# Kernel tuning notes

Hardware: AMD Instinct MI355X
Metric: run time of the kernel (lower is better)

Reference implementation:

```python
import jax, jax.numpy as jnp
import numpy as np

D = 1024

def setup_inputs() -> dict:
    key = jax.random.key(0)
    ks = jax.random.split(key, 16)
    B, S = 8, 2048
    s = 1.0 / np.sqrt(D)
    inp = {
        "visual_feat": jax.random.normal(ks[0], (B, S, D), jnp.float32),
        "audio_feat": jax.random.normal(ks[1], (B, S, D), jnp.float32),
        "Wq": jax.random.normal(ks[2], (D, D), jnp.float32) * s,
        "bq": jnp.zeros((D,), jnp.float32),
        "Wk": jax.random.normal(ks[3], (D, D), jnp.float32) * s,
        "bk": jnp.zeros((D,), jnp.float32),
        "Wv": jax.random.normal(ks[4], (D, D), jnp.float32) * s,
        "bv": jnp.zeros((D,), jnp.float32),
        "Wo": jax.random.normal(ks[5], (D, D), jnp.float32) * s,
        "bo": jnp.zeros((D,), jnp.float32),
        "W1": jax.random.normal(ks[6], (D, D), jnp.float32) * s,
        "b1": jnp.zeros((D,), jnp.float32),
        "W2": jax.random.normal(ks[7], (D, 1), jnp.float32) * s,
        "b2": jnp.zeros((1,), jnp.float32),
    }
    return inp

def reference(visual_feat, audio_feat, Wq, bq, Wk, bk, Wv, bv, Wo, bo, W1, b1, W2, b2):
    # Cross-modal attention: query from visual, key/value from audio.
    q = jnp.einsum('bsd,de->bse', visual_feat, Wq) + bq
    k = jnp.einsum('bsd,de->bse', audio_feat, Wk) + bk
    v = jnp.einsum('bsd,de->bse', audio_feat, Wv) + bv
    # NOTE: original has NO 1/sqrt(d) scaling — faithful to source.
    scores = jnp.einsum('bqe,bke->bqk', q, k)          # [B, S, S]
    attn = jax.nn.softmax(scores, axis=-1)
    attended = jnp.einsum('bqk,bke->bqe', attn, v)     # [B, S, D]
    attended = jnp.einsum('bse,ef->bsf', attended, Wo) + bo
    h = attended + visual_feat                          # residual
    x = jax.nn.relu(jnp.einsum('bsd,de->bse', h, W1) + b1)
    out = jnp.einsum('bsd,do->bso', x, W2) + b2        # [B, S, 1]
    return out
```

## Files before the change

kernel.cpp:

```cpp
#include <hip/hip_runtime.h>
#include <cstdint>
#include <cstddef>

typedef _Float16 f16;
typedef _Float16 f16x8 __attribute__((ext_vector_type(8)));
typedef _Float16 f16x4 __attribute__((ext_vector_type(4)));
typedef float    f32x4 __attribute__((ext_vector_type(4)));

#define AS1 __attribute__((address_space(1)))
#define AS3 __attribute__((address_space(3)))

static constexpr int BB = 8;
static constexpr int SS = 2048;
static constexpr int DD = 1024;
static constexpr int MTOT = BB * SS;

__global__ __launch_bounds__(256) void cast_f32_f16(const float* __restrict__ src,
                                                    f16* __restrict__ dst, int n4) {
  int i = blockIdx.x * 256 + threadIdx.x;
  if (i < n4) {
    const float4 f = reinterpret_cast<const float4*>(src)[i];
    f16x4 o = { (f16)f.x, (f16)f.y, (f16)f.z, (f16)f.w };
    reinterpret_cast<f16x4*>(dst)[i] = o;
  }
}

__global__ __launch_bounds__(256) void transpose_cast_wt(const float* __restrict__ W,
                                                         f16* __restrict__ WT, int D) {
  __shared__ float tile[32][33];
  const int bx = blockIdx.x * 32;
  const int by = blockIdx.y * 32;
  const int tx = threadIdx.x & 31;
  const int ty = threadIdx.x >> 5;
  for (int i = ty; i < 32; i += 8) tile[i][tx] = W[(size_t)(by + i) * D + bx + tx];
  __syncthreads();
  for (int i = ty; i < 32; i += 8)
    WT[(size_t)(bx + i) * D + by + tx] = (f16)tile[tx][i];
}

__global__ __launch_bounds__(256) void transpose_f16_batch(const f16* __restrict__ src,
                                                           f16* __restrict__ dst,
                                                           int R, int C) {
  __shared__ f16 tile[32][33];
  src += (size_t)blockIdx.z * R * C;
  dst += (size_t)blockIdx.z * R * C;
  const int bx = blockIdx.x * 32;
  const int by = blockIdx.y * 32;
  const int tx = threadIdx.x & 31;
  const int ty = threadIdx.x >> 5;
  for (int i = ty; i < 32; i += 8) tile[i][tx] = src[(size_t)(by + i) * C + bx + tx];
  __syncthreads();
  for (int i = ty; i < 32; i += 8) dst[(size_t)(bx + i) * R + by + tx] = tile[tx][i];
}

template <int EPI>
__global__ __launch_bounds__(512, 2) void gemm8(
    const f16* __restrict__ A, const f16* __restrict__ BT, void* __restrict__ Cout,
    const float* __restrict__ bias, const float* __restrict__ resid,
    int N, int K, int gx,
    size_t Abat, size_t Bbat, size_t Cbat) {
  __shared__ f16 smA[2][256 * 64];
  __shared__ f16 smB[2][256 * 64];

  const int bz = blockIdx.z;
  A += (size_t)bz * Abat;
  BT += (size_t)bz * Bbat;

  const int nwg = gridDim.x;
  const int q = nwg >> 3, r = nwg & 7;
  const int xcd = blockIdx.x & 7, lin = blockIdx.x >> 3;
  const int wg = (xcd < r ? xcd * (q + 1) : r * (q + 1) + (xcd - r) * q) + lin;
  const int n0 = (wg % gx) * 256;
  const int m0 = (wg / gx) * 256;

  const int tid = threadIdx.x;
  const int w = tid >> 6, lane = tid & 63;
  const int wr = w >> 2, wc = w & 3;
  const int lg = lane >> 4, lr = lane & 15;
  const int nt = K >> 6;

  f32x4 acc[8][4] = {};
  f16x8 alo[4][2], ahi[4][2], bfr[2][2];

  auto stageA = [&](int t, int h, int d) {
#pragma unroll
    for (int l = 0; l < 2; ++l) {
      const int cb = l * 512 + w * 64;
      const int c = cb + lane;
      const int rr = c >> 3;
      const int g = (c & 7) ^ (rr & 7);
      const f16* src = A + (size_t)(m0 + h * 128 + rr) * K + t * 64 + g * 8;
      __builtin_amdgcn_global_load_lds((const AS1 void*)src,
          (AS3 void*)(&smA[d][(h * 1024 + cb) * 8]), 16, 0, 0);
    }
  };
  auto stageB = [&](int t, int h, int d) {
#pragma unroll
    for (int l = 0; l < 2; ++l) {
      const int cb = l * 512 + w * 64;
      const int c = cb + lane;
      const int rr = c >> 3;
      const int g = (c & 7) ^ (rr & 7);
      const f16* src = BT + (size_t)(n0 + h * 128 + rr) * K + t * 64 + g * 8;
      __builtin_amdgcn_global_load_lds((const AS1 void*)src,
          (AS3 void*)(&smB[d][(h * 1024 + cb) * 8]), 16, 0, 0);
    }
  };
  auto lda = [&](f16x8 (&dst)[4][2], int mh, int d) {
#pragma unroll
    for (int i = 0; i < 4; ++i) {
      const int rrow = wr * 128 + (mh * 4 + i) * 16 + lr;
#pragma unroll
      for (int kh = 0; kh < 2; ++kh) {
        const int kg = (kh * 4 + lg) ^ (rrow & 7);
        dst[i][kh] = *(const f16x8*)(&smA[d][rrow * 64 + kg * 8]);
      }
    }
  };
  auto ldb = [&](int nh, int d) {
#pragma unroll
    for (int j = 0; j < 2; ++j) {
      const int nrow = wc * 64 + (nh * 2 + j) * 16 + lr;
#pragma unroll
      for (int kh = 0; kh < 2; ++kh) {
        const int kg = (kh * 4 + lg) ^ (nrow & 7);
        bfr[j][kh] = *(const f16x8*)(&smB[d][nrow * 64 + kg * 8]);
      }
    }
  };
  auto mma = [&](const f16x8 (&a)[4][2], int mh, int nh) {
#pragma unroll
    for (int i = 0; i < 4; ++i)
#pragma unroll
      for (int j = 0; j < 2; ++j)
#pragma unroll
        for (int kh = 0; kh < 2; ++kh)
          acc[mh * 4 + i][nh * 2 + j] = __builtin_amdgcn_mfma_f32_16x16x32_f16(
              a[i][kh], bfr[j][kh], acc[mh * 4 + i][nh * 2 + j], 0, 0, 0);
  };

#define PH_MID()                                                     \
  __builtin_amdgcn_sched_barrier(0);                                 \
  __builtin_amdgcn_s_barrier();                                      \
  asm volatile("s_waitcnt lgkmcnt(0)" ::: "memory");                 \
  __builtin_amdgcn_sched_barrier(0);                                 \
  __builtin_amdgcn_s_setprio(1)
#define PH_END()                                                     \
  __builtin_amdgcn_s_setprio(0);                                     \
  __builtin_amdgcn_sched_barrier(0);                                 \
  __builtin_amdgcn_s_barrier()
#define PH_END_VM4()                                                 \
  __builtin_amdgcn_s_setprio(0);                                     \
  asm volatile("s_waitcnt vmcnt(4)" ::: "memory");                   \
  __builtin_amdgcn_sched_barrier(0);                                 \
  __builtin_amdgcn_s_barrier()
#define PH_END_VM0()                                                 \
  __builtin_amdgcn_s_setprio(0);                                     \
  asm volatile("s_waitcnt vmcnt(0)" ::: "memory");                   \
  __builtin_amdgcn_sched_barrier(0);                                 \
  __builtin_amdgcn_s_barrier()

  stageA(0, 0, 0); stageA(0, 1, 0);
  stageB(0, 0, 0); stageB(0, 1, 0);
  if (nt > 1) { stageA(1, 0, 1); stageA(1, 1, 1); }
  asm volatile("s_waitcnt vmcnt(4)" ::: "memory");
  __builtin_amdgcn_sched_barrier(0);
  __builtin_amdgcn_s_barrier();

  for (int t = 0; t < nt; t += 2) {
    const int u = t + 1;
    const bool pok = (t + 2 < nt);
    lda(alo, 0, 0); ldb(0, 0); stageB(u, 0, 1);
    PH_MID(); mma(alo, 0, 0); PH_END();
    lda(ahi, 1, 0); stageB(u, 1, 1);
    PH_MID(); mma(ahi, 1, 0); PH_END();
    ldb(1, 0); if (pok) stageA(t + 2, 0, 0);
    PH_MID(); mma(ahi, 1, 1); PH_END();
    if (pok) stageA(t + 2, 1, 0);
    PH_MID(); mma(alo, 0, 1);
    if (pok) { PH_END_VM4(); } else { PH_END_VM0(); }
    lda(alo, 0, 1); ldb(0, 1); if (pok) stageB(t + 2, 0, 0);
    PH_MID(); mma(alo, 0, 0); PH_END();
    lda(ahi, 1, 1); if (pok) stageB(t + 2, 1, 0);
    PH_MID(); mma(ahi, 1, 0); PH_END();
    ldb(1, 1); if (pok) stageA(t + 3, 0, 1);
    PH_MID(); mma(ahi, 1, 1); PH_END();
    if (pok) stageA(t + 3, 1, 1);
    PH_MID(); mma(alo, 0, 1);
    if (pok) { PH_END_VM4(); } else { PH_END(); }
  }
#undef PH_MID
#undef PH_END
#undef PH_END_VM4
#undef PH_END_VM0

#pragma unroll
  for (int I = 0; I < 8; ++I) {
    const int row = m0 + wr * 128 + I * 16 + lg * 4;
#pragma unroll
    for (int J = 0; J < 4; ++J) {
      const int col = n0 + wc * 64 + J * 16 + lr;
      float bval = 0.f;
      if (EPI == 0 || EPI == 3 || EPI == 4) bval = bias[col];
#pragma unroll
      for (int rr = 0; rr < 4; ++rr) {
        float v = acc[I][J][rr] + bval;
        const size_t idx = (size_t)(row + rr) * N + col;
        if (EPI == 3) v += resid[idx];
        if (EPI == 4) v = fmaxf(v, 0.f);
        if (EPI == 1)
          ((float*)Cout)[(size_t)bz * Cbat + idx] = v;
        else
          ((f16*)Cout)[(size_t)bz * Cbat + idx] = (f16)v;
      }
    }
  }
}

__global__ __launch_bounds__(256) void softmax_rows(const float* __restrict__ Sc,
                                                    f16* __restrict__ P) {
  const size_t row = blockIdx.x;
  const float* x = Sc + row * SS;
  f16* p = P + row * SS;
  const int t = threadIdx.x;
  const int wid = t >> 6, lane = t & 63;
  __shared__ float red[8];

  float v[8];
  float mx = -3.4e38f;
#pragma unroll
  for (int i = 0; i < 8; ++i) {
    v[i] = x[t + i * 256];
    mx = fmaxf(mx, v[i]);
  }
#pragma unroll
  for (int o = 32; o >= 1; o >>= 1) mx = fmaxf(mx, __shfl_xor(mx, o));
  if (lane == 0) red[wid] = mx;
  __syncthreads();
  mx = fmaxf(fmaxf(red[0], red[1]), fmaxf(red[2], red[3]));

  float sum = 0.f;
#pragma unroll
  for (int i = 0; i < 8; ++i) {
    v[i] = __expf(v[i] - mx);
    sum += v[i];
  }
#pragma unroll
  for (int o = 32; o >= 1; o >>= 1) sum += __shfl_xor(sum, o);
  if (lane == 0) red[4 + wid] = sum;
  __syncthreads();
  sum = red[4] + red[5] + red[6] + red[7];
  const float inv = 1.0f / sum;
#pragma unroll
  for (int i = 0; i < 8; ++i) p[t + i * 256] = (f16)(v[i] * inv);
}

__global__ __launch_bounds__(256) void matvec_out(const f16* __restrict__ X,
                                                  const float* __restrict__ W2,
                                                  const float* __restrict__ b2,
                                                  float* __restrict__ out) {
  const int row = blockIdx.x * 4 + (threadIdx.x >> 6);
  const int lane = threadIdx.x & 63;
  const f16* x = X + (size_t)row * DD;
  float s = 0.f;
#pragma unroll
  for (int c = 0; c < 2; ++c) {
    const int base = lane * 8 + c * 512;
    f16x8 v = *(const f16x8*)(x + base);
#pragma unroll
    for (int e = 0; e < 8; ++e) s += (float)v[e] * W2[base + e];
  }
#pragma unroll
  for (int o = 32; o >= 1; o >>= 1) s += __shfl_xor(s, o);
  if (lane == 0) out[row] = s + b2[0];
}

extern "C" void kernel_launch(void* const* d_in, const int* in_sizes, int n_in,
                              void* d_out, int out_size, void* d_ws, size_t ws_size,
                              hipStream_t stream) {
  const float* vis = (const float*)d_in[0];
  const float* aud = (const float*)d_in[1];
  const float* Wq = (const float*)d_in[2];
  const float* bq = (const float*)d_in[3];
  const float* Wk = (const float*)d_in[4];
  const float* bk = (const float*)d_in[5];
  const float* Wv = (const float*)d_in[6];
  const float* bv = (const float*)d_in[7];
  const float* Wo = (const float*)d_in[8];
  const float* bo = (const float*)d_in[9];
  const float* W1 = (const float*)d_in[10];
  const float* b1 = (const float*)d_in[11];
  const float* W2 = (const float*)d_in[12];
  const float* b2 = (const float*)d_in[13];
  float* out = (float*)d_out;
  (void)in_sizes; (void)n_in; (void)out_size;

  char* ws = (char*)d_ws;
  size_t off = 0;
  auto carve = [&](size_t bytes) -> void* {
    void* p = ws + off;
    off += (bytes + 255) & ~(size_t)255;
    return p;
  };
  const size_t wtB = (size_t)DD * DD * sizeof(f16);
  const size_t bufB = (size_t)MTOT * DD * sizeof(f16);
  f16* WqT = (f16*)carve(wtB);
  f16* WkT = (f16*)carve(wtB);
  f16* WvT = (f16*)carve(wtB);
  f16* WoT = (f16*)carve(wtB);
  f16* W1T = (f16*)carve(wtB);
  f16* slot1 = (f16*)carve(bufB);
  f16* slot2 = (f16*)carve(bufB);
  f16* slot3 = (f16*)carve(bufB);
  f16* slot4 = (f16*)carve(bufB);

  const size_t rem = (ws_size > off) ? ws_size - off : 0;
  const size_t perBatch = (size_t)SS * SS * 6 + 512;
  int nb = 0;
  for (int c : {8, 4, 2, 1})
    if ((size_t)c * perBatch <= rem) { nb = c; break; }
  int RB = 0;
  if (!nb) {
    for (int r : {1024, 512, 256})
      if ((size_t)r * SS * 6 + 512 <= rem) { RB = r; break; }
    if (!RB) RB = 256;
  }

  f16* VIS16 = slot1;
  f16* AUD16 = slot2;
  f16* Q16 = slot3;
  f16* K16 = slot4;
  f16* V16 = slot1;
  f16* VT16 = slot2;
  f16* ATT16 = slot1;
  f16* H16 = slot2;
  f16* X16 = slot3;

  const dim3 blk(256);
  const dim3 blk8(512);
  const int n4 = MTOT * DD / 4;

  cast_f32_f16<<<dim3((n4 + 255) / 256), blk, 0, stream>>>(vis, VIS16, n4);
  cast_f32_f16<<<dim3((n4 + 255) / 256), blk, 0, stream>>>(aud, AUD16, n4);

  transpose_cast_wt<<<dim3(DD / 32, DD / 32), blk, 0, stream>>>(Wq, WqT, DD);
  transpose_cast_wt<<<dim3(DD / 32, DD / 32), blk, 0, stream>>>(Wk, WkT, DD);
  transpose_cast_wt<<<dim3(DD / 32, DD / 32), blk, 0, stream>>>(Wv, WvT, DD);
  transpose_cast_wt<<<dim3(DD / 32, DD / 32), blk, 0, stream>>>(Wo, WoT, DD);
  transpose_cast_wt<<<dim3(DD / 32, DD / 32), blk, 0, stream>>>(W1, W1T, DD);

  gemm8<0><<<dim3(4 * 64, 1, 1), blk8, 0, stream>>>(
      VIS16, WqT, Q16, bq, nullptr, DD, DD, 4, 0, 0, 0);
  gemm8<0><<<dim3(4 * 64, 1, 1), blk8, 0, stream>>>(
      AUD16, WkT, K16, bk, nullptr, DD, DD, 4, 0, 0, 0);
  gemm8<0><<<dim3(4 * 64, 1, 1), blk8, 0, stream>>>(
      AUD16, WvT, V16, bv, nullptr, DD, DD, 4, 0, 0, 0);

  transpose_f16_batch<<<dim3(DD / 32, SS / 32, BB), blk, 0, stream>>>(V16, VT16, SS, DD);

  if (nb) {
    float* S32 = (float*)carve((size_t)nb * SS * SS * sizeof(float));
    f16* Pc = (f16*)carve((size_t)nb * SS * SS * sizeof(f16));
    for (int b = 0; b < BB; b += nb) {
      gemm8<1><<<dim3((SS / 256) * (SS / 256), 1, nb), blk8, 0, stream>>>(
          Q16 + (size_t)b * SS * DD, K16 + (size_t)b * SS * DD, S32, nullptr, nullptr,
          SS, DD, SS / 256, (size_t)SS * DD, (size_t)SS * DD, (size_t)SS * SS);
      softmax_rows<<<dim3(nb * SS), blk, 0, stream>>>(S32, Pc);
      gemm8<2><<<dim3((DD / 256) * (SS / 256), 1, nb), blk8, 0, stream>>>(
          Pc, VT16 + (size_t)b * DD * SS, ATT16 + (size_t)b * SS * DD, nullptr, nullptr,
          DD, SS, DD / 256, (size_t)SS * SS, (size_t)DD * SS, (size_t)SS * DD);
    }
  } else {
    float* S32 = (float*)carve((size_t)RB * SS * sizeof(float));
    f16* Pc = (f16*)carve((size_t)RB * SS * sizeof(f16));
    for (int b = 0; b < BB; ++b) {
      for (int r0 = 0; r0 < SS; r0 += RB) {
        gemm8<1><<<dim3((SS / 256) * (RB / 256), 1, 1), blk8, 0, stream>>>(
            Q16 + ((size_t)b * SS + r0) * DD, K16 + (size_t)b * SS * DD, S32,
            nullptr, nullptr, SS, DD, SS / 256, 0, 0, 0);
        softmax_rows<<<dim3(RB), blk, 0, stream>>>(S32, Pc);
        gemm8<2><<<dim3((DD / 256) * (RB / 256), 1, 1), blk8, 0, stream>>>(
            Pc, VT16 + (size_t)b * DD * SS, ATT16 + ((size_t)b * SS + r0) * DD,
            nullptr, nullptr, DD, SS, DD / 256, 0, 0, 0);
      }
    }
  }

  gemm8<3><<<dim3(4 * 64, 1, 1), blk8, 0, stream>>>(
      ATT16, WoT, H16, bo, vis, DD, DD, 4, 0, 0, 0);

  gemm8<4><<<dim3(4 * 64, 1, 1), blk8, 0, stream>>>(
      H16, W1T, X16, b1, nullptr, DD, DD, 4, 0, 0, 0);

  matvec_out<<<dim3(MTOT / 4), blk, 0, stream>>>(X16, W2, b2, out);
}
```

Before: 553.2 us.

## Fuse W2 matvec into W1 GEMM epilogue and batch attention PV GEMM

The W1 GEMM epilogue now applies bias and ReLU, multiplies by W2, reduces across 16-lane groups, and writes per-64-column partial sums. A small reduce kernel then adds the partials and b2, so the f16 X buffer is never written or read back. The attention path now runs two 4-batch QK/softmax passes into separate P buffers and a single 8-batch PV GEMM, using a split A pointer. This cuts launches and gives the PV GEMM more parallelism, but it needs more workspace and drops the intermediate nb/RB fallback sizes.

```diff
diff --git a/kernel.cpp b/kernel.cpp
--- a/kernel.cpp
+++ b/kernel.cpp
@@ -55,7 +55,8 @@
 
 template <int EPI>
 __global__ __launch_bounds__(512, 2) void gemm8(
-    const f16* __restrict__ A, const f16* __restrict__ BT, void* __restrict__ Cout,
+    const f16* __restrict__ A, const f16* __restrict__ A2, int zsplit,
+    const f16* __restrict__ BT, void* __restrict__ Cout,
     const float* __restrict__ bias, const float* __restrict__ resid,
     int N, int K, int gx,
     size_t Abat, size_t Bbat, size_t Cbat) {
@@ -63,7 +64,8 @@
   __shared__ f16 smB[2][256 * 64];
 
   const int bz = blockIdx.z;
-  A += (size_t)bz * Abat;
+  const f16* Ab = (zsplit && bz >= zsplit) ? A2 + (size_t)(bz - zsplit) * Abat
+                                           : A + (size_t)bz * Abat;
   BT += (size_t)bz * Bbat;
 
   const int nwg = gridDim.x;
@@ -89,7 +91,7 @@
       const int c = cb + lane;
       const int rr = c >> 3;
       const int g = (c & 7) ^ (rr & 7);
-      const f16* src = A + (size_t)(m0 + h * 128 + rr) * K + t * 64 + g * 8;
+      const f16* src = Ab + (size_t)(m0 + h * 128 + rr) * K + t * 64 + g * 8;
       __builtin_amdgcn_global_load_lds((const AS1 void*)src,
           (AS3 void*)(&smA[d][(h * 1024 + cb) * 8]), 16, 0, 0);
     }
@@ -194,6 +196,30 @@
 #undef PH_END_VM4
 #undef PH_END_VM0
 
+  if (EPI == 4) {
+    float* part = (float*)Cout;
+    const int cq = (n0 >> 6) + wc;
+#pragma unroll
+    for (int I = 0; I < 8; ++I) {
+#pragma unroll
+      for (int rr = 0; rr < 4; ++rr) {
+        const int row = m0 + wr * 128 + I * 16 + lg * 4 + rr;
+        float s = 0.f;
+#pragma unroll
+        for (int J = 0; J < 4; ++J) {
+          const int col = n0 + wc * 64 + J * 16 + lr;
+          float v = acc[I][J][rr] + bias[col];
+          v = fmaxf(v, 0.f);
+          s += v * resid[col];
+        }
+#pragma unroll
+        for (int o = 1; o < 16; o <<= 1) s += __shfl_xor(s, o);
+        if (lr == 0) part[(size_t)cq * MTOT + row] = s;
+      }
+    }
+    return;
+  }
+
 #pragma unroll
   for (int I = 0; I < 8; ++I) {
     const int row = m0 + wr * 128 + I * 16 + lg * 4;
@@ -201,13 +227,12 @@
     for (int J = 0; J < 4; ++J) {
       const int col = n0 + wc * 64 + J * 16 + lr;
       float bval = 0.f;
-      if (EPI == 0 || EPI == 3 || EPI == 4) bval = bias[col];
+      if (EPI == 0 || EPI == 3) bval = bias[col];
 #pragma unroll
       for (int rr = 0; rr < 4; ++rr) {
         float v = acc[I][J][rr] + bval;
         const size_t idx = (size_t)(row + rr) * N + col;
         if (EPI == 3) v += resid[idx];
-        if (EPI == 4) v = fmaxf(v, 0.f);
         if (EPI == 1)
           ((float*)Cout)[(size_t)bz * Cbat + idx] = v;
         else
@@ -255,24 +280,14 @@
   for (int i = 0; i < 8; ++i) p[t + i * 256] = (f16)(v[i] * inv);
 }
 
-__global__ __launch_bounds__(256) void matvec_out(const f16* __restrict__ X,
-                                                  const float* __restrict__ W2,
+__global__ __launch_bounds__(256) void reduce_out(const float* __restrict__ part,
                                                   const float* __restrict__ b2,
                                                   float* __restrict__ out) {
-  const int row = blockIdx.x * 4 + (threadIdx.x >> 6);
-  const int lane = threadIdx.x & 63;
-  const f16* x = X + (size_t)row * DD;
+  const int i = blockIdx.x * 256 + threadIdx.x;
   float s = 0.f;
 #pragma unroll
-  for (int c = 0; c < 2; ++c) {
-    const int base = lane * 8 + c * 512;
-    f16x8 v = *(const f16x8*)(x + base);
-#pragma unroll
-    for (int e = 0; e < 8; ++e) s += (float)v[e] * W2[base + e];
-  }
-#pragma unroll
-  for (int o = 32; o >= 1; o >>= 1) s += __shfl_xor(s, o);
-  if (lane == 0) out[row] = s + b2[0];
+  for (int c = 0; c < 16; ++c) s += part[(size_t)c * MTOT + i];
+  out[i] = s + b2[0];
 }
 
 extern "C" void kernel_launch(void* const* d_in, const int* in_sizes, int n_in,
@@ -315,16 +330,7 @@
   f16* slot4 = (f16*)carve(bufB);
 
   const size_t rem = (ws_size > off) ? ws_size - off : 0;
-  const size_t perBatch = (size_t)SS * SS * 6 + 512;
-  int nb = 0;
-  for (int c : {8, 4, 2, 1})
-    if ((size_t)c * perBatch <= rem) { nb = c; break; }
-  int RB = 0;
-  if (!nb) {
-    for (int r : {1024, 512, 256})
-      if ((size_t)r * SS * 6 + 512 <= rem) { RB = r; break; }
-    if (!RB) RB = 256;
-  }
+  const size_t needMain = (size_t)4 * SS * SS * 4 + (size_t)4 * SS * SS * 2 + 512;
 
   f16* VIS16 = slot1;
   f16* AUD16 = slot2;
@@ -333,8 +339,9 @@
   f16* V16 = slot1;
   f16* VT16 = slot2;
   f16* ATT16 = slot1;
-  f16* H16 = slot2;
-  f16* X16 = slot3;
+  f16* P1 = slot3;
+  f16* H16 = slot3;
+  float* partials = (float*)slot4;
 
   const dim3 blk(256);
   const dim3 blk8(512);
@@ -350,47 +357,52 @@
   transpose_cast_wt<<<dim3(DD / 32, DD / 32), blk, 0, stream>>>(W1, W1T, DD);
 
   gemm8<0><<<dim3(4 * 64, 1, 1), blk8, 0, stream>>>(
-      VIS16, WqT, Q16, bq, nullptr, DD, DD, 4, 0, 0, 0);
+      VIS16, nullptr, 0, WqT, Q16, bq, nullptr, DD, DD, 4, 0, 0, 0);
   gemm8<0><<<dim3(4 * 64, 1, 1), blk8, 0, stream>>>(
-      AUD16, WkT, K16, bk, nullptr, DD, DD, 4, 0, 0, 0);
+      AUD16, nullptr, 0, WkT, K16, bk, nullptr, DD, DD, 4, 0, 0, 0);
   gemm8<0><<<dim3(4 * 64, 1, 1), blk8, 0, stream>>>(
-      AUD16, WvT, V16, bv, nullptr, DD, DD, 4, 0, 0, 0);
+      AUD16, nullptr, 0, WvT, V16, bv, nullptr, DD, DD, 4, 0, 0, 0);
 
   transpose_f16_batch<<<dim3(DD / 32, SS / 32, BB), blk, 0, stream>>>(V16, VT16, SS, DD);
 
-  if (nb) {
-    float* S32 = (float*)carve((size_t)nb * SS * SS * sizeof(float));
-    f16* Pc = (f16*)carve((size_t)nb * SS * SS * sizeof(f16));
-    for (int b = 0; b < BB; b += nb) {
-      gemm8<1><<<dim3((SS / 256) * (SS / 256), 1, nb), blk8, 0, stream>>>(
-          Q16 + (size_t)b * SS * DD, K16 + (size_t)b * SS * DD, S32, nullptr, nullptr,
-          SS, DD, SS / 256, (size_t)SS * DD, (size_t)SS * DD, (size_t)SS * SS);
-      softmax_rows<<<dim3(nb * SS), blk, 0, stream>>>(S32, Pc);
-      gemm8<2><<<dim3((DD / 256) * (SS / 256), 1, nb), blk8, 0, stream>>>(
-          Pc, VT16 + (size_t)b * DD * SS, ATT16 + (size_t)b * SS * DD, nullptr, nullptr,
-          DD, SS, DD / 256, (size_t)SS * SS, (size_t)DD * SS, (size_t)SS * DD);
-    }
+  if (rem >= needMain) {
+    float* S32 = (float*)carve((size_t)4 * SS * SS * sizeof(float));
+    f16* P0 = (f16*)carve((size_t)4 * SS * SS * sizeof(f16));
+    gemm8<1><<<dim3((SS / 256) * (SS / 256), 1, 4), blk8, 0, stream>>>(
+        Q16, nullptr, 0, K16, S32, nullptr, nullptr,
+        SS, DD, SS / 256, (size_t)SS * DD, (size_t)SS * DD, (size_t)SS * SS);
+    softmax_rows<<<dim3(4 * SS), blk, 0, stream>>>(S32, P0);
+    gemm8<1><<<dim3((SS / 256) * (SS / 256), 1, 4), blk8, 0, stream>>>(
+        Q16 + (size_t)4 * SS * DD, nullptr, 0, K16 + (size_t)4 * SS * DD, S32,
+        nullptr, nullptr, SS, DD, SS / 256,
+        (size_t)SS * DD, (size_t)SS * DD, (size_t)SS * SS);
+    softmax_rows<<<dim3(4 * SS), blk, 0, stream>>>(S32, P1);
+    gemm8<2><<<dim3((DD / 256) * (SS / 256), 1, 8), blk8, 0, stream>>>(
+        P0, P1, 4, VT16, ATT16, nullptr, nullptr,
+        DD, SS, DD / 256, (size_t)SS * SS, (size_t)DD * SS, (size_t)SS * DD);
   } else {
+    const int RB = 256;
     float* S32 = (float*)carve((size_t)RB * SS * sizeof(float));
     f16* Pc = (f16*)carve((size_t)RB * SS * sizeof(f16));
     for (int b = 0; b < BB; ++b) {
       for (int r0 = 0; r0 < SS; r0 += RB) {
         gemm8<1><<<dim3((SS / 256) * (RB / 256), 1, 1), blk8, 0, stream>>>(
-            Q16 + ((size_t)b * SS + r0) * DD, K16 + (size_t)b * SS * DD, S32,
-            nullptr, nullptr, SS, DD, SS / 256, 0, 0, 0);
+            Q16 + ((size_t)b * SS + r0) * DD, nullptr, 0, K16 + (size_t)b * SS * DD,
+            S32, nullptr, nullptr, SS, DD, SS / 256, 0, 0, 0);
         softmax_rows<<<dim3(RB), blk, 0, stream>>>(S32, Pc);
         gemm8<2><<<dim3((DD / 256) * (RB / 256), 1, 1), blk8, 0, stream>>>(
-            Pc, VT16 + (size_t)b * DD * SS, ATT16 + ((size_t)b * SS + r0) * DD,
-            nullptr, nullptr, DD, SS, DD / 256, 0, 0, 0);
+            Pc, nullptr, 0, VT16 + (size_t)b * DD * SS,
+            ATT16 + ((size_t)b * SS + r0) * DD, nullptr, nullptr,
+            DD, SS, DD / 256, 0, 0, 0);
       }
     }
   }
 
   gemm8<3><<<dim3(4 * 64, 1, 1), blk8, 0, stream>>>(
-      ATT16, WoT, H16, bo, vis, DD, DD, 4, 0, 0, 0);
+      ATT16, nullptr, 0, WoT, H16, bo, vis, DD, DD, 4, 0, 0, 0);
 
   gemm8<4><<<dim3(4 * 64, 1, 1), blk8, 0, stream>>>(
-      H16, W1T, X16, b1, nullptr, DD, DD, 4, 0, 0, 0);
-
-  matvec_out<<<dim3(MTOT / 4), blk, 0, stream>>>(X16, W2, b2, out);
-}
+      H16, nullptr, 0, W1T, partials, b1, W2, DD, DD, 4, 0, 0, 0);
+
+  reduce_out<<<dim3(MTOT / 256), blk, 0, stream>>>(partials, b2, out);
+}
```

New measurement: 486.8 us. 12.0% less time.
